# Kernel optimization log

Hardware: AMD Instinct MI355X
Metric: run time of the kernel (lower is better)

## Reference

```python
import jax, jax.numpy as jnp
import numpy as np

B, N, D_IN = 4, 2048, 768
D_OUT, H = 768, 12
HD = D_OUT // H  # 64


def setup_inputs() -> dict:
    key = jax.random.key(0)
    ks = jax.random.split(key, 6)
    s = 0.02
    return {
        "x": jax.random.normal(ks[0], (B, N, D_IN), dtype=jnp.float32),
        "W_q": jax.random.normal(ks[1], (D_IN, D_OUT), dtype=jnp.float32) * s,
        "W_k": jax.random.normal(ks[2], (D_IN, D_OUT), dtype=jnp.float32) * s,
        "W_v": jax.random.normal(ks[3], (D_IN, D_OUT), dtype=jnp.float32) * s,
        "W_o": jax.random.normal(ks[4], (D_OUT, D_OUT), dtype=jnp.float32) * s,
        "b_o": jax.random.normal(ks[5], (D_OUT,), dtype=jnp.float32) * s,
    }


def reference(x, W_q, W_k, W_v, W_o, b_o):
    b, n, _ = x.shape
    # project and split heads: [b, h, n, hd]
    q = (x @ W_q).reshape(b, n, H, HD).transpose(0, 2, 1, 3)
    k = (x @ W_k).reshape(b, n, H, HD).transpose(0, 2, 1, 3)
    v = (x @ W_v).reshape(b, n, H, HD).transpose(0, 2, 1, 3)
    scores = jnp.einsum("bhqd,bhkd->bhqk", q, k)
    causal = jnp.tril(jnp.ones((n, n), dtype=bool))
    scores = jnp.where(causal, scores, -jnp.inf)
    w = jax.nn.softmax(scores / jnp.sqrt(jnp.float32(HD)), axis=-1)
    ctx = jnp.einsum("bhqk,bhkd->bhqd", w, v)
    ctx = ctx.transpose(0, 2, 1, 3).reshape(b, n, D_OUT)
    return ctx @ W_o + b_o
```

## Files before the change

kernel.cpp:

```cpp
#include <hip/hip_runtime.h>
#include <hip/hip_bf16.h>
#include <stdint.h>

typedef unsigned short u16;
typedef __attribute__((ext_vector_type(8))) short short8;
typedef __attribute__((ext_vector_type(4))) float f32x4;
typedef __attribute__((ext_vector_type(16))) float f32x16;

#define GLOBAL_AS __attribute__((address_space(1)))
#define LDS_AS __attribute__((address_space(3)))

#define BB 4
#define NSEQ 2048
#define DIN 768
#define DOUT 768
#define NH 12
#define HD 64
#define MROWS (BB*NSEQ)

static __device__ __forceinline__ u16 f2bf(float f) {
  union { float f; uint32_t u; } v; v.f = f;
  uint32_t r = (v.u + 0x7fffu + ((v.u >> 16) & 1u)) >> 16;
  return (u16)r;
}
static __device__ __forceinline__ uint32_t pack2b(float lo, float hi) {
  union { __hip_bfloat162 h; uint32_t u; } cv;
  cv.h.x = __float2bfloat16(lo);
  cv.h.y = __float2bfloat16(hi);
  return cv.u;
}

__global__ __launch_bounds__(256) void convert2_k(const float* __restrict__ x,
                          const float* __restrict__ Wq, const float* __restrict__ Wk,
                          const float* __restrict__ Wv, const float* __restrict__ Wo,
                          u16* __restrict__ xb, u16* __restrict__ WqT,
                          u16* __restrict__ WkT, u16* __restrict__ WvT,
                          u16* __restrict__ WoT) {
  int tid = threadIdx.x;
  if (blockIdx.x < 576) {
    int wi = blockIdx.x;
    int which = wi / 144, t = wi % 144;
    int tr = t / 12, tc = t % 12;
    const float* src = which==0 ? Wq : which==1 ? Wk : which==2 ? Wv : Wo;
    u16* dst = which==0 ? WqT : which==1 ? WkT : which==2 ? WvT : WoT;
    __shared__ u16 lt[64][65];
    int r0 = tid >> 6, c = tid & 63;
#pragma unroll
    for (int rr=0; rr<16; rr++) {
      int row = rr*4 + r0;
      lt[row][c] = f2bf(src[(size_t)(tr*64+row)*DOUT + tc*64 + c]);
    }
    __syncthreads();
#pragma unroll
    for (int rr=0; rr<16; rr++) {
      int row = rr*4 + r0;
      dst[(size_t)(tc*64+row)*DIN + tr*64 + c] = lt[c][row];
    }
  } else {
    const float4* x4 = (const float4*)x;
    uint2* o4 = (uint2*)xb;
    int n4 = MROWS*DIN/4;
    int i = (int)(blockIdx.x - 576) * 256 + tid;
    for (; i < n4; i += 2048*256) {
      float4 v = x4[i];
      uint2 o; o.x = pack2b(v.x, v.y); o.y = pack2b(v.z, v.w);
      o4[i] = o;
    }
  }
}

__global__ __launch_bounds__(256) void gemm_qkv_k(const u16* __restrict__ A,
                                                  const u16* __restrict__ Bt,
                                                  u16* __restrict__ Qg,
                                                  u16* __restrict__ Kgo,
                                                  u16* __restrict__ Vto) {
  const int K = DIN;
  int xcd = blockIdx.x & 7, j = blockIdx.x >> 3;
  int m0 = (xcd*8 + (j & 7)) * 128;
  int nt = j >> 3;
  nt = (nt % 3) * 6 + nt / 3;
  int n0 = nt * 128;
  int tid = threadIdx.x;
  int lane = tid & 63, wid = tid >> 6;
  int wr = wid >> 1, wc = wid & 1;
  int g = lane >> 4, r = lane & 15;

  __shared__ __attribute__((aligned(16))) u16 sbuf[128*129];
  u16* lA = sbuf;
  u16* lB = sbuf + 8192;

  int srow0 = (wid*2)*16 + (lane >> 2);
  int sslot = (lane & 3) ^ ((lane >> 2) & 3);
  auto stage = [&](int buf, int k0) {
#pragma unroll
    for (int i=0;i<2;i++) {
      int ch = wid*2 + i;
      int row = srow0 + i*16;
      __builtin_amdgcn_global_load_lds(
        (GLOBAL_AS void*)(A + (size_t)(m0+row)*K + k0 + sslot*8),
        (LDS_AS void*)(&lA[buf*4096 + ch*512 + (lane&63)*8]), 16, 0, 0);
      __builtin_amdgcn_global_load_lds(
        (GLOBAL_AS void*)(Bt + (size_t)(n0+row)*K + k0 + sslot*8),
        (LDS_AS void*)(&lB[buf*4096 + ch*512 + (lane&63)*8]), 16, 0, 0);
    }
  };

  f32x4 acc[4][4];
#pragma unroll
  for (int i=0;i<4;i++)
#pragma unroll
    for (int jj=0;jj<4;jj++) acc[i][jj] = (f32x4){0.f,0.f,0.f,0.f};

  int rsw = (r & 3);
  auto compute = [&](int buf, int k0) {
    short8 af[4], bf[4];
#pragma unroll
    for (int f=0; f<4; f++) {
      af[f] = *(const short8*)&lA[buf*4096 + (wr*64 + f*16 + r)*32 + ((g ^ rsw)*8)];
      bf[f] = *(const short8*)&lB[buf*4096 + (wc*64 + f*16 + r)*32 + ((g ^ rsw)*8)];
    }
#pragma unroll
    for (int fr=0; fr<4; fr++)
#pragma unroll
      for (int fc=0; fc<4; fc++)
        acc[fr][fc] = __builtin_amdgcn_mfma_f32_16x16x32_bf16(af[fr], bf[fc], acc[fr][fc], 0, 0, 0);
  };

  stage(0, 0);
  for (int k0 = 0; k0 < K; k0 += 64) {
    asm volatile("s_waitcnt vmcnt(0)" ::: "memory");
    __builtin_amdgcn_s_barrier();
    asm volatile("" ::: "memory");
    stage(1, k0 + 32);
    compute(0, k0);
    asm volatile("s_waitcnt vmcnt(0)" ::: "memory");
    __builtin_amdgcn_s_barrier();
    asm volatile("" ::: "memory");
    if (k0 + 64 < K) stage(0, k0 + 64);
    compute(1, k0 + 32);
  }
  __syncthreads();

  if (n0 < 1536) {
    bool isQ = n0 < 768;
    u16* outb = isQ ? Qg : Kgo;
    int nb = isQ ? n0 : n0 - 768;
#pragma unroll
    for (int fr=0; fr<4; fr++)
#pragma unroll
      for (int fc=0; fc<4; fc++)
#pragma unroll
        for (int v=0; v<4; v++) {
          int row = m0 + wr*64 + fr*16 + g*4 + v;
          int cc  = nb + wc*64 + fc*16 + r;
          int b = row >> 11, nn = row & (NSEQ-1);
          float val = acc[fr][fc][v];
          if (isQ) val *= 0.18033688f;
          outb[(((size_t)b*NH + (cc>>6))*NSEQ + nn)*HD + (cc&63)] = f2bf(val);
        }
  } else {
    int nb = n0 - 1536;
#pragma unroll
    for (int fr=0; fr<4; fr++)
#pragma unroll
      for (int fc=0; fc<4; fc++)
#pragma unroll
        for (int v=0; v<4; v++) {
          int ii = wr*64 + fr*16 + g*4 + v;
          int jj = wc*64 + fc*16 + r;
          sbuf[ii*129 + jj] = f2bf(acc[fr][fc][v]);
        }
    __syncthreads();
    int b = m0 >> 11;
#pragma unroll 1
    for (int rep=0; rep<64; rep++) {
      int flat = rep*256 + tid;
      int jj = flat >> 7, ii = flat & 127;
      int cc = nb + jj;
      int nn = (m0 + ii) & (NSEQ-1);
      Vto[(((size_t)b*NH + (cc>>6))*HD + (cc&63))*NSEQ + nn] = sbuf[ii*129 + jj];
    }
  }
}

__global__ __launch_bounds__(256) void gemm_o_k(const u16* __restrict__ A,
                                                const u16* __restrict__ Bt,
                                                float* __restrict__ outf,
                                                const float* __restrict__ bias) {
  const int K = DIN;
  int xcd = blockIdx.x & 7, j = blockIdx.x >> 3;
  int m0 = (xcd*8 + (j & 7)) * 128;
  int n0 = (j >> 3) * 128;
  int tid = threadIdx.x;
  int lane = tid & 63, wid = tid >> 6;
  int wr = wid >> 1, wc = wid & 1;
  int g = lane >> 4, r = lane & 15;

  __shared__ __attribute__((aligned(16))) u16 lA[2][4096];
  __shared__ __attribute__((aligned(16))) u16 lB[2][4096];

  int srow0 = (wid*2)*16 + (lane >> 2);
  int sslot = (lane & 3) ^ ((lane >> 2) & 3);
  auto stage = [&](int buf, int k0) {
#pragma unroll
    for (int i=0;i<2;i++) {
      int ch = wid*2 + i;
      int row = srow0 + i*16;
      __builtin_amdgcn_global_load_lds(
        (GLOBAL_AS void*)(A + (size_t)(m0+row)*K + k0 + sslot*8),
        (LDS_AS void*)(&lA[buf][ch*512 + (lane&63)*8]), 16, 0, 0);
      __builtin_amdgcn_global_load_lds(
        (GLOBAL_AS void*)(Bt + (size_t)(n0+row)*K + k0 + sslot*8),
        (LDS_AS void*)(&lB[buf][ch*512 + (lane&63)*8]), 16, 0, 0);
    }
  };

  f32x4 acc[4][4];
#pragma unroll
  for (int i=0;i<4;i++)
#pragma unroll
    for (int jj=0;jj<4;jj++) acc[i][jj] = (f32x4){0.f,0.f,0.f,0.f};

  int rsw = (r & 3);
  auto compute = [&](int buf, int k0) {
    short8 af[4], bf[4];
#pragma unroll
    for (int f=0; f<4; f++) {
      af[f] = *(const short8*)&lA[buf][(wr*64 + f*16 + r)*32 + ((g ^ rsw)*8)];
      bf[f] = *(const short8*)&lB[buf][(wc*64 + f*16 + r)*32 + ((g ^ rsw)*8)];
    }
#pragma unroll
    for (int fr=0; fr<4; fr++)
#pragma unroll
      for (int fc=0; fc<4; fc++)
        acc[fr][fc] = __builtin_amdgcn_mfma_f32_16x16x32_bf16(af[fr], bf[fc], acc[fr][fc], 0, 0, 0);
  };

  stage(0, 0);
  for (int k0 = 0; k0 < K; k0 += 64) {
    asm volatile("s_waitcnt vmcnt(0)" ::: "memory");
    __builtin_amdgcn_s_barrier();
    asm volatile("" ::: "memory");
    stage(1, k0 + 32);
    compute(0, k0);
    asm volatile("s_waitcnt vmcnt(0)" ::: "memory");
    __builtin_amdgcn_s_barrier();
    asm volatile("" ::: "memory");
    if (k0 + 64 < K) stage(0, k0 + 64);
    compute(1, k0 + 32);
  }

#pragma unroll
  for (int fr=0; fr<4; fr++)
#pragma unroll
    for (int fc=0; fc<4; fc++)
#pragma unroll
      for (int v=0; v<4; v++) {
        int row = m0 + wr*64 + fr*16 + g*4 + v;
        int cc  = n0 + wc*64 + fc*16 + r;
        outf[(size_t)row*DOUT + cc] = acc[fr][fc][v] + bias[cc];
      }
}

__global__ __launch_bounds__(256, 4) void attn8_k(const u16* __restrict__ Q,
                                                  const u16* __restrict__ Kg,
                                                  const u16* __restrict__ Vt,
                                                  u16* __restrict__ ctx) {
  int i = blockIdx.x;
  int xcd = i & 7, j = i >> 3;
  int bh = xcd * 6 + (j >> 5);
  int chunk = 31 - (j & 31);
  int nkt = chunk + 1;
  int lane = threadIdx.x & 63;
  int w = threadIdx.x >> 6;
  int p = w >> 1;
  int ch = w & 1;
  int col = lane & 31;
  int hi = lane >> 5;
  int sw = (col & 7) << 4;

  const u16* Qb = Q  + (size_t)bh * NSEQ * HD;
  const u16* Kb = Kg + (size_t)bh * NSEQ * HD;
  const u16* Vb = Vt + (size_t)bh * HD * NSEQ;

  __shared__ __attribute__((aligned(16))) char smem[2][16384];

  auto stage = [&](int buf, int k0) {
#pragma unroll
    for (int ii=0; ii<2; ii++) {
      int cb = (w*2+ii) * 1024;
      int d  = cb + lane*16;
      int row = d >> 7;
      int src = (d & 127) ^ ((row & 7) << 4);
      __builtin_amdgcn_global_load_lds(
        (GLOBAL_AS void*)((const char*)Kb + (size_t)(k0+row)*128 + src),
        (LDS_AS void*)(&smem[buf][cb]), 16, 0, 0);
      __builtin_amdgcn_global_load_lds(
        (GLOBAL_AS void*)((const char*)Vb + (size_t)row*(NSEQ*2) + (size_t)k0*2 + src),
        (LDS_AS void*)(&smem[buf][8192+cb]), 16, 0, 0);
    }
  };

  int qw0 = chunk*64 + p*32;
  int q = qw0 + col;

  short8 qf[4];
#pragma unroll
  for (int ksl = 0; ksl < 4; ksl++)
    qf[ksl] = *(const short8*)&Qb[(size_t)q * HD + ksl*16 + hi*8];

  short8 ones8;
#pragma unroll
  for (int z=0; z<8; z++) ones8[z] = (short)0x3F80;

  f32x16 od[2], ol;
#pragma unroll
  for (int z=0; z<16; z++) { od[0][z] = 0.f; od[1][z] = 0.f; ol[z] = 0.f; }

  stage(0, 0);

#pragma unroll 1
  for (int t = 0; t < nkt; t++) {
    asm volatile("s_waitcnt vmcnt(0)" ::: "memory");
    __builtin_amdgcn_s_barrier();
    asm volatile("" ::: "memory");

    if (t + 1 < nkt) stage((t+1) & 1, (t+1)*64);

    int k0c = t*64 + ch*32;
    if (k0c <= qw0 + 31) {
      const char* Kt = &smem[t & 1][0];
      const char* Vtile = &smem[t & 1][8192];
      f32x16 s;
#pragma unroll
      for (int z=0; z<16; z++) s[z] = 0.f;
#pragma unroll
      for (int ksl=0; ksl<4; ksl++) {
        short8 kf = *(const short8*)(Kt + (ch*32+col)*128 + ((ksl*32 + hi*16) ^ sw));
        s = __builtin_amdgcn_mfma_f32_32x32x16_bf16(kf, qf[ksl], s, 0, 0, 0);
      }
      if (k0c + 31 > qw0) {
#pragma unroll
        for (int r2=0; r2<16; r2++) {
          int kv = k0c + (r2&3) + 8*(r2>>2) + 4*hi;
          if (kv > q) s[r2] = -1e30f;
        }
      }
      uint32_t a[8];
#pragma unroll
      for (int ww=0; ww<8; ww++) {
        float p0 = __builtin_amdgcn_exp2f(s[2*ww]);
        float p1 = __builtin_amdgcn_exp2f(s[2*ww+1]);
        a[ww] = pack2b(p0, p1);
      }

      uint32_t w0=a[0], w2=a[2], w1=a[1], w3=a[3];
      asm volatile("v_permlane32_swap_b32 %0, %1" : "+v"(w0), "+v"(w2));
      asm volatile("v_permlane32_swap_b32 %0, %1" : "+v"(w1), "+v"(w3));
      uint32_t w4=a[4], w6=a[6], w5=a[5], w7=a[7];
      asm volatile("v_permlane32_swap_b32 %0, %1" : "+v"(w4), "+v"(w6));
      asm volatile("v_permlane32_swap_b32 %0, %1" : "+v"(w5), "+v"(w7));
      union { uint32_t wdat[4]; short8 s8; } u0, u1;
      u0.wdat[0]=w0; u0.wdat[1]=w1; u0.wdat[2]=w2; u0.wdat[3]=w3;
      u1.wdat[0]=w4; u1.wdat[1]=w5; u1.wdat[2]=w6; u1.wdat[3]=w7;

#pragma unroll
      for (int dc=0; dc<2; dc++) {
        short8 vf0 = *(const short8*)(Vtile + (dc*32+col)*128 + ((ch*64 + hi*16) ^ sw));
        od[dc] = __builtin_amdgcn_mfma_f32_32x32x16_bf16(vf0, u0.s8, od[dc], 0, 0, 0);
        short8 vf1 = *(const short8*)(Vtile + (dc*32+col)*128 + ((ch*64 + 32 + hi*16) ^ sw));
        od[dc] = __builtin_amdgcn_mfma_f32_32x32x16_bf16(vf1, u1.s8, od[dc], 0, 0, 0);
      }
      ol = __builtin_amdgcn_mfma_f32_32x32x16_bf16(ones8, u0.s8, ol, 0, 0, 0);
      ol = __builtin_amdgcn_mfma_f32_32x32x16_bf16(ones8, u1.s8, ol, 0, 0, 0);
    }
  }
  __syncthreads();

  float* mg = (float*)&smem[0][0] + p * (33*64);
  if (ch) {
#pragma unroll
    for (int dc=0; dc<2; dc++)
#pragma unroll
      for (int jj=0; jj<16; jj++) mg[(dc*16+jj)*64 + lane] = od[dc][jj];
    mg[32*64 + lane] = ol[0];
  }
  __syncthreads();
  if (!ch) {
    float inv = 1.0f / (ol[0] + mg[32*64 + lane]);
    int b = bh / NH, h = bh % NH;
    u16* cp_ = ctx + ((size_t)b * NSEQ + q) * DOUT + h * HD;
#pragma unroll
    for (int dc=0; dc<2; dc++)
#pragma unroll
      for (int t4=0; t4<4; t4++) {
        int d0 = dc*32 + t4*8 + hi*4;
        float v0 = (od[dc][t4*4+0] + mg[(dc*16+t4*4+0)*64 + lane]) * inv;
        float v1 = (od[dc][t4*4+1] + mg[(dc*16+t4*4+1)*64 + lane]) * inv;
        float v2 = (od[dc][t4*4+2] + mg[(dc*16+t4*4+2)*64 + lane]) * inv;
        float v3 = (od[dc][t4*4+3] + mg[(dc*16+t4*4+3)*64 + lane]) * inv;
        *(uint32_t*)(cp_ + d0)     = pack2b(v0, v1);
        *(uint32_t*)(cp_ + d0 + 2) = pack2b(v2, v3);
      }
  }
}

extern "C" void kernel_launch(void* const* d_in, const int* in_sizes, int n_in,
                              void* d_out, int out_size, void* d_ws, size_t ws_size,
                              hipStream_t stream) {
  const float* x   = (const float*)d_in[0];
  const float* Wq  = (const float*)d_in[1];
  const float* Wk  = (const float*)d_in[2];
  const float* Wv  = (const float*)d_in[3];
  const float* Wo  = (const float*)d_in[4];
  const float* bo  = (const float*)d_in[5];
  float* out = (float*)d_out;

  u16* ws  = (u16*)d_ws;
  u16* xb  = ws;
  u16* WqT = xb  + (size_t)MROWS*DIN;
  u16* WkT = WqT + (size_t)DIN*DOUT;
  u16* WvT = WkT + (size_t)DIN*DOUT;
  u16* WoT = WvT + (size_t)DIN*DOUT;
  u16* Qg  = WoT + (size_t)DIN*DOUT;
  u16* Kg  = Qg  + (size_t)MROWS*DOUT;
  u16* Vt  = Kg  + (size_t)MROWS*DOUT;
  u16* ctx = Vt  + (size_t)MROWS*DOUT;

  convert2_k<<<2624, 256, 0, stream>>>(x, Wq, Wk, Wv, Wo, xb, WqT, WkT, WvT, WoT);

  gemm_qkv_k<<<1152, 256, 0, stream>>>(xb, WqT, Qg, Kg, Vt);

  attn8_k<<<1536, 256, 0, stream>>>(Qg, Kg, Vt, ctx);

  gemm_o_k<<<384, 256, 0, stream>>>(ctx, WoT, out, bo);
}
```

Measured before the change: 132.4 us.

## Triple-buffer GEMM K-loop with partial vmcnt waits and drop LDS swizzle

Both projection GEMMs move from a double-buffered LDS pipeline that waited on all outstanding loads (vmcnt(0)) to a three-stage ring. It waits only until the oldest stage has landed (vmcnt(4)), so two tiles stay in flight while one is computed. The XOR slot swizzle on staging and fragment reads is removed in favour of a plain row-major layout, which saves index arithmetic but may bring back LDS bank conflicts. The loop issues redundant dummy loads at the tail, and the O GEMM has no final vmcnt(0) drain before the epilogue.

```diff
diff --git a/kernel.cpp b/kernel.cpp
--- a/kernel.cpp
+++ b/kernel.cpp
@@ -85,23 +85,22 @@
   int wr = wid >> 1, wc = wid & 1;
   int g = lane >> 4, r = lane & 15;
 
-  __shared__ __attribute__((aligned(16))) u16 sbuf[128*129];
-  u16* lA = sbuf;
-  u16* lB = sbuf + 8192;
-
-  int srow0 = (wid*2)*16 + (lane >> 2);
-  int sslot = (lane & 3) ^ ((lane >> 2) & 3);
-  auto stage = [&](int buf, int k0) {
+  __shared__ __attribute__((aligned(16))) u16 sbuf[24576];
+
+  auto stage = [&](int bi, int k0) {
+    u16* dA = sbuf + bi*4096;
+    u16* dB = sbuf + 12288 + bi*4096;
 #pragma unroll
     for (int i=0;i<2;i++) {
       int ch = wid*2 + i;
-      int row = srow0 + i*16;
-      __builtin_amdgcn_global_load_lds(
-        (GLOBAL_AS void*)(A + (size_t)(m0+row)*K + k0 + sslot*8),
-        (LDS_AS void*)(&lA[buf*4096 + ch*512 + (lane&63)*8]), 16, 0, 0);
-      __builtin_amdgcn_global_load_lds(
-        (GLOBAL_AS void*)(Bt + (size_t)(n0+row)*K + k0 + sslot*8),
-        (LDS_AS void*)(&lB[buf*4096 + ch*512 + (lane&63)*8]), 16, 0, 0);
+      int e = ch*512 + lane*8;
+      int row = e >> 5, col = e & 31;
+      __builtin_amdgcn_global_load_lds(
+        (GLOBAL_AS void*)(A + (size_t)(m0+row)*K + k0 + col),
+        (LDS_AS void*)(&dA[ch*512]), 16, 0, 0);
+      __builtin_amdgcn_global_load_lds(
+        (GLOBAL_AS void*)(Bt + (size_t)(n0+row)*K + k0 + col),
+        (LDS_AS void*)(&dB[ch*512]), 16, 0, 0);
     }
   };
 
@@ -111,13 +110,14 @@
 #pragma unroll
     for (int jj=0;jj<4;jj++) acc[i][jj] = (f32x4){0.f,0.f,0.f,0.f};
 
-  int rsw = (r & 3);
-  auto compute = [&](int buf, int k0) {
+  auto compute = [&](int bi, int k0) {
+    const u16* sA = sbuf + bi*4096;
+    const u16* sB = sbuf + 12288 + bi*4096;
     short8 af[4], bf[4];
 #pragma unroll
     for (int f=0; f<4; f++) {
-      af[f] = *(const short8*)&lA[buf*4096 + (wr*64 + f*16 + r)*32 + ((g ^ rsw)*8)];
-      bf[f] = *(const short8*)&lB[buf*4096 + (wc*64 + f*16 + r)*32 + ((g ^ rsw)*8)];
+      af[f] = *(const short8*)&sA[(wr*64 + f*16 + r)*32 + g*8];
+      bf[f] = *(const short8*)&sB[(wc*64 + f*16 + r)*32 + g*8];
     }
 #pragma unroll
     for (int fr=0; fr<4; fr++)
@@ -127,18 +127,27 @@
   };
 
   stage(0, 0);
-  for (int k0 = 0; k0 < K; k0 += 64) {
-    asm volatile("s_waitcnt vmcnt(0)" ::: "memory");
-    __builtin_amdgcn_s_barrier();
-    asm volatile("" ::: "memory");
-    stage(1, k0 + 32);
+  stage(1, 32);
+  for (int k0 = 0; k0 < K; k0 += 96) {
+    asm volatile("s_waitcnt vmcnt(4)" ::: "memory");
+    __builtin_amdgcn_s_barrier();
+    asm volatile("" ::: "memory");
+    stage(2, k0 + 64);
     compute(0, k0);
-    asm volatile("s_waitcnt vmcnt(0)" ::: "memory");
-    __builtin_amdgcn_s_barrier();
-    asm volatile("" ::: "memory");
-    if (k0 + 64 < K) stage(0, k0 + 64);
+
+    asm volatile("s_waitcnt vmcnt(4)" ::: "memory");
+    __builtin_amdgcn_s_barrier();
+    asm volatile("" ::: "memory");
+    { int kn = k0 + 96;  stage(0, kn < K ? kn : 0); }
     compute(1, k0 + 32);
-  }
+
+    asm volatile("s_waitcnt vmcnt(4)" ::: "memory");
+    __builtin_amdgcn_s_barrier();
+    asm volatile("" ::: "memory");
+    { int kn = k0 + 128; stage(1, kn < K ? kn : 32); }
+    compute(2, k0 + 64);
+  }
+  asm volatile("s_waitcnt vmcnt(0)" ::: "memory");
   __syncthreads();
 
   if (n0 < 1536) {
@@ -196,22 +205,23 @@
   int wr = wid >> 1, wc = wid & 1;
   int g = lane >> 4, r = lane & 15;
 
-  __shared__ __attribute__((aligned(16))) u16 lA[2][4096];
-  __shared__ __attribute__((aligned(16))) u16 lB[2][4096];
-
-  int srow0 = (wid*2)*16 + (lane >> 2);
-  int sslot = (lane & 3) ^ ((lane >> 2) & 3);
-  auto stage = [&](int buf, int k0) {
+  __shared__ __attribute__((aligned(16))) u16 lA[3*4096];
+  __shared__ __attribute__((aligned(16))) u16 lB[3*4096];
+
+  auto stage = [&](int bi, int k0) {
+    u16* dA = lA + bi*4096;
+    u16* dB = lB + bi*4096;
 #pragma unroll
     for (int i=0;i<2;i++) {
       int ch = wid*2 + i;
-      int row = srow0 + i*16;
-      __builtin_amdgcn_global_load_lds(
-        (GLOBAL_AS void*)(A + (size_t)(m0+row)*K + k0 + sslot*8),
-        (LDS_AS void*)(&lA[buf][ch*512 + (lane&63)*8]), 16, 0, 0);
-      __builtin_amdgcn_global_load_lds(
-        (GLOBAL_AS void*)(Bt + (size_t)(n0+row)*K + k0 + sslot*8),
-        (LDS_AS void*)(&lB[buf][ch*512 + (lane&63)*8]), 16, 0, 0);
+      int e = ch*512 + lane*8;
+      int row = e >> 5, col = e & 31;
+      __builtin_amdgcn_global_load_lds(
+        (GLOBAL_AS void*)(A + (size_t)(m0+row)*K + k0 + col),
+        (LDS_AS void*)(&dA[ch*512]), 16, 0, 0);
+      __builtin_amdgcn_global_load_lds(
+        (GLOBAL_AS void*)(Bt + (size_t)(n0+row)*K + k0 + col),
+        (LDS_AS void*)(&dB[ch*512]), 16, 0, 0);
     }
   };
 
@@ -221,13 +231,14 @@
 #pragma unroll
     for (int jj=0;jj<4;jj++) acc[i][jj] = (f32x4){0.f,0.f,0.f,0.f};
 
-  int rsw = (r & 3);
-  auto compute = [&](int buf, int k0) {
+  auto compute = [&](int bi, int k0) {
+    const u16* sA = lA + bi*4096;
+    const u16* sB = lB + bi*4096;
     short8 af[4], bf[4];
 #pragma unroll
     for (int f=0; f<4; f++) {
-      af[f] = *(const short8*)&lA[buf][(wr*64 + f*16 + r)*32 + ((g ^ rsw)*8)];
-      bf[f] = *(const short8*)&lB[buf][(wc*64 + f*16 + r)*32 + ((g ^ rsw)*8)];
+      af[f] = *(const short8*)&sA[(wr*64 + f*16 + r)*32 + g*8];
+      bf[f] = *(const short8*)&sB[(wc*64 + f*16 + r)*32 + g*8];
     }
 #pragma unroll
     for (int fr=0; fr<4; fr++)
@@ -237,17 +248,25 @@
   };
 
   stage(0, 0);
-  for (int k0 = 0; k0 < K; k0 += 64) {
-    asm volatile("s_waitcnt vmcnt(0)" ::: "memory");
-    __builtin_amdgcn_s_barrier();
-    asm volatile("" ::: "memory");
-    stage(1, k0 + 32);
+  stage(1, 32);
+  for (int k0 = 0; k0 < K; k0 += 96) {
+    asm volatile("s_waitcnt vmcnt(4)" ::: "memory");
+    __builtin_amdgcn_s_barrier();
+    asm volatile("" ::: "memory");
+    stage(2, k0 + 64);
     compute(0, k0);
-    asm volatile("s_waitcnt vmcnt(0)" ::: "memory");
-    __builtin_amdgcn_s_barrier();
-    asm volatile("" ::: "memory");
-    if (k0 + 64 < K) stage(0, k0 + 64);
+
+    asm volatile("s_waitcnt vmcnt(4)" ::: "memory");
+    __builtin_amdgcn_s_barrier();
+    asm volatile("" ::: "memory");
+    { int kn = k0 + 96;  stage(0, kn < K ? kn : 0); }
     compute(1, k0 + 32);
+
+    asm volatile("s_waitcnt vmcnt(4)" ::: "memory");
+    __builtin_amdgcn_s_barrier();
+    asm volatile("" ::: "memory");
+    { int kn = k0 + 128; stage(1, kn < K ? kn : 32); }
+    compute(2, k0 + 64);
   }
 
 #pragma unroll
```

Result: faster. 127.0 us, median of 2 (-4.1%).
